# Kernel tuning notes

Measured on AMD Instinct MI355X. Metric: run time of the kernel, lower is better.

## Reference

```python
import jax, jax.numpy as jnp
import numpy as np

B, T, D = 16, 1024, 1024
H, HS = 16, 64  # num_heads, attention_head_size; H*HS == D
NEG_INF = -1e9


def setup_inputs() -> dict:
    key = jax.random.key(0)
    ks = jax.random.split(key, 6)
    s = 0.02
    x = jax.random.normal(ks[0], (B, T, D), dtype=jnp.float32)
    Wq = jax.random.normal(ks[1], (D, HS), dtype=jnp.float32) * s
    Wk = jax.random.normal(ks[2], (D, HS), dtype=jnp.float32) * s
    Wv = jax.random.normal(ks[3], (D, HS), dtype=jnp.float32) * s
    Wp = jax.random.normal(ks[4], (D, D), dtype=jnp.float32) * s
    bp = jax.random.normal(ks[5], (D,), dtype=jnp.float32) * s
    return {"x": x, "Wq": Wq, "Wk": Wk, "Wv": Wv, "Wp": Wp, "bp": bp}


def reference(x, Wq, Wk, Wv, Wp, bp):
    # Single shared Head (ModuleList([Head(...)] * num_heads) shares weights).
    q = jnp.einsum('btd,dh->bth', x, Wq)  # [B,T,HS]
    k = jnp.einsum('btd,dh->bth', x, Wk)
    v = jnp.einsum('btd,dh->bth', x, Wv)
    scale = 1.0 / jnp.sqrt(jnp.float32(HS))
    scores = jnp.einsum('bth,bsh->bts', q, k) * scale  # [B,T,T]
    causal = jnp.tril(jnp.ones((T, T), dtype=bool))
    scores = jnp.where(causal[None, :, :], scores, NEG_INF)
    attn = jax.nn.softmax(scores, axis=-1)
    head_out = jnp.einsum('bts,bsh->bth', attn, v)  # [B,T,HS]
    # Concatenate H identical head outputs along feature dim -> [B,T,D]
    out = jnp.tile(head_out, (1, 1, H))
    out = jnp.einsum('btd,de->bte', out, Wp) + bp
    return out
```

## Files before the change

### kernel.cpp

```cpp
#include <hip/hip_runtime.h>
#include <hip/hip_bf16.h>
#include <cstddef>

typedef __attribute__((ext_vector_type(8))) __bf16 bf16x8;
typedef __attribute__((ext_vector_type(4))) float f32x4;

static __device__ __forceinline__ unsigned short f2bf(float f) {
    __bf16 h = (__bf16)f;
    return __builtin_bit_cast(unsigned short, h);
}

__global__ void prep_weights(const float* __restrict__ Wq, const float* __restrict__ Wk,
                             const float* __restrict__ Wv, const float* __restrict__ Wp,
                             unsigned short* __restrict__ Wfrag,
                             unsigned short* __restrict__ WpFrag) {
    int blk = blockIdx.x;
    if (blk < 768) {
        int idx = blk * 256 + threadIdx.x;
        int CB = idx >> 14;
        int rem = idx & 16383;
        int S = rem >> 9;
        int r2 = rem & 511;
        int l = r2 >> 3, j = r2 & 7;
        int col = CB * 16 + (l & 15);
        int k = S * 32 + (l >> 4) * 8 + j;
        float v;
        if (col < 64)       v = Wq[k * 64 + col];
        else if (col < 128) v = Wk[k * 64 + (col - 64)];
        else                v = Wv[k * 64 + (col - 128)];
        Wfrag[idx] = f2bf(v);
    } else {
        int idx = (blk - 768) * 256 + threadIdx.x;
        int CB = idx >> 10;
        int rem = idx & 1023;
        int s = rem >> 9;
        int r2 = rem & 511;
        int l = r2 >> 3, j = r2 & 7;
        int col = CB * 16 + (l & 15);
        int h = s * 32 + (l >> 4) * 8 + j;
        float sum = 0.f;
#pragma unroll
        for (int j16 = 0; j16 < 16; ++j16) sum += Wp[(size_t)(j16 * 64 + h) * 1024 + col];
        WpFrag[idx] = f2bf(sum);
    }
}

__global__ __launch_bounds__(256) void qkv_gemm(const float* __restrict__ x,
                                                const unsigned short* __restrict__ Wfrag,
                                                unsigned short* __restrict__ qs,
                                                unsigned short* __restrict__ ks,
                                                unsigned short* __restrict__ vT) {
    __shared__ __align__(16) unsigned short xl[2][16 * 128];

    const int tid = threadIdx.x;
    const int lane = tid & 63;
    const int w = tid >> 6;
    const int g = lane >> 4, c = lane & 15;
    const int row0 = blockIdx.x * 16;

    const int srow = tid >> 4;
    const int scolf = (tid & 15) * 8;
    const float* xsrc = x + (size_t)(row0 + srow) * 1024 + scolf;
    const int sdst = srow * 256 + ((scolf * 2) ^ ((srow & 7) << 4));

    const unsigned short* wbase = Wfrag + (size_t)(w * 3) * 32 * 512 + lane * 8;

    f32x4 acc[3];
#pragma unroll
    for (int cb = 0; cb < 3; ++cb) acc[cb] = (f32x4){0.f, 0.f, 0.f, 0.f};

    float4 pre0[2], pre1[2];
    pre0[0] = *(const float4*)(xsrc);
    pre0[1] = *(const float4*)(xsrc + 4);
    pre1[0] = *(const float4*)(xsrc + 128);
    pre1[1] = *(const float4*)(xsrc + 132);

    bf16x8 bP[3][6];
#pragma unroll
    for (int pp = 0; pp < 2; ++pp) {
#pragma unroll
        for (int i = 0; i < 6; ++i) {
            int SB = pp * 2 + (i / 3);
            int cb = i % 3;
            bP[pp][i] = *(const bf16x8*)(wbase + ((size_t)(cb * 32 + SB) * 512));
        }
    }

    {
        bf16x8 vv;
        vv[0] = (__bf16)pre0[0].x; vv[1] = (__bf16)pre0[0].y; vv[2] = (__bf16)pre0[0].z; vv[3] = (__bf16)pre0[0].w;
        vv[4] = (__bf16)pre0[1].x; vv[5] = (__bf16)pre0[1].y; vv[6] = (__bf16)pre0[1].z; vv[7] = (__bf16)pre0[1].w;
        *(bf16x8*)((char*)xl[0] + sdst) = vv;
    }
    __syncthreads();

#pragma unroll
    for (int p = 0; p < 16; ++p) {
        const int t = p >> 1;
        if ((p & 1) == 0 && t + 2 < 8) {
            if ((t & 1) == 0) {
                pre0[0] = *(const float4*)(xsrc + (t + 2) * 128);
                pre0[1] = *(const float4*)(xsrc + (t + 2) * 128 + 4);
            } else {
                pre1[0] = *(const float4*)(xsrc + (t + 2) * 128);
                pre1[1] = *(const float4*)(xsrc + (t + 2) * 128 + 4);
            }
        }
        if (p + 2 < 16) {
#pragma unroll
            for (int i = 0; i < 6; ++i) {
                int SB = (p + 2) * 2 + (i / 3);
                int cb = i % 3;
                bP[(p + 2) % 3][i] = *(const bf16x8*)(wbase + ((size_t)(cb * 32 + SB) * 512));
            }
        }
#pragma unroll
        for (int sl = 0; sl < 2; ++sl) {
            int s = (p & 1) * 2 + sl;
            bf16x8 af = *(const bf16x8*)((char*)xl[t & 1] + c * 256 +
                                         ((s * 64 + g * 16) ^ ((c & 7) << 4)));
#pragma unroll
            for (int cb = 0; cb < 3; ++cb)
                acc[cb] = __builtin_amdgcn_mfma_f32_16x16x32_bf16(af, bP[p % 3][sl * 3 + cb], acc[cb], 0, 0, 0);
        }
        if (p & 1) {
            if (t < 7) {
                bf16x8 vv;
                if ((t & 1) == 0) {
                    vv[0] = (__bf16)pre1[0].x; vv[1] = (__bf16)pre1[0].y; vv[2] = (__bf16)pre1[0].z; vv[3] = (__bf16)pre1[0].w;
                    vv[4] = (__bf16)pre1[1].x; vv[5] = (__bf16)pre1[1].y; vv[6] = (__bf16)pre1[1].z; vv[7] = (__bf16)pre1[1].w;
                    *(bf16x8*)((char*)xl[1] + sdst) = vv;
                } else {
                    vv[0] = (__bf16)pre0[0].x; vv[1] = (__bf16)pre0[0].y; vv[2] = (__bf16)pre0[0].z; vv[3] = (__bf16)pre0[0].w;
                    vv[4] = (__bf16)pre0[1].x; vv[5] = (__bf16)pre0[1].y; vv[6] = (__bf16)pre0[1].z; vv[7] = (__bf16)pre0[1].w;
                    *(bf16x8*)((char*)xl[0] + sdst) = vv;
                }
            }
            __syncthreads();
        }
    }

    const float QSCALE = 0.125f * 1.44269504088896340736f;
#pragma unroll
    for (int cb = 0; cb < 3; ++cb) {
        int col = w * 48 + cb * 16 + c;
        int rowb = row0 + g * 4;
        if (col < 64) {
#pragma unroll
            for (int r = 0; r < 4; ++r)
                qs[(size_t)(rowb + r) * 64 + col] = f2bf(acc[cb][r] * QSCALE);
        } else if (col < 128) {
#pragma unroll
            for (int r = 0; r < 4; ++r)
                ks[(size_t)(rowb + r) * 64 + (col - 64)] = f2bf(acc[cb][r]);
        } else {
            int h = col - 128;
            int b = rowb >> 10, trow = rowb & 1023;
            unsigned long long dv =
                (unsigned long long)f2bf(acc[cb][0]) |
                ((unsigned long long)f2bf(acc[cb][1]) << 16) |
                ((unsigned long long)f2bf(acc[cb][2]) << 32) |
                ((unsigned long long)f2bf(acc[cb][3]) << 48);
            *(unsigned long long*)(vT + (size_t)b * 65536 + (size_t)h * 1024 + trow) = dv;
        }
    }
}

__global__ __launch_bounds__(256) void attn_proj(const unsigned short* __restrict__ qs,
                                                 const unsigned short* __restrict__ ks,
                                                 const unsigned short* __restrict__ vT,
                                                 const unsigned short* __restrict__ WpFrag,
                                                 const float* __restrict__ bp,
                                                 float* __restrict__ out) {
    __shared__ unsigned short Plds[4][16 * 40];
    __shared__ float oL[3][1024];
    __shared__ float pL[3][256];
    __shared__ __align__(16) unsigned short hl[16 * 64];

    const int tid = threadIdx.x;
    const int lane = tid & 63;
    const int q4 = tid >> 6;
    const int g = lane >> 4, c = lane & 15;

    const int tau = blockIdx.x;
    const int b = tau & 15;
    const int qidx = 63 - (tau >> 4);
    const int qr0 = qidx * 16;
    const int qend = qr0 + 16;
    const int nc = (qidx >> 1) + 1;
    const int c0 = (q4 * nc) >> 2;
    const int c1 = ((q4 + 1) * nc) >> 2;

    const unsigned short* qbase = qs + ((size_t)b * 1024 + qr0 + c) * 64 + g * 8;
    bf16x8 aq0 = *(const bf16x8*)(qbase);
    bf16x8 aq1 = *(const bf16x8*)(qbase + 32);

    const unsigned short* kB = ks + (size_t)b * 1024 * 64;
    const unsigned short* vB = vT + (size_t)b * 64 * 1024;

    f32x4 o[4];
#pragma unroll
    for (int i = 0; i < 4; ++i) o[i] = (f32x4){0.f, 0.f, 0.f, 0.f};
    float psum[4] = {0.f, 0.f, 0.f, 0.f};
    const f32x4 zero = {0.f, 0.f, 0.f, 0.f};

    bf16x8 kc0, kc1, kc2, kc3, vc0, vc1, vc2, vc3;
    if (c0 < c1) {
        const unsigned short* kp = kB + (size_t)(c0 * 32 + c) * 64 + g * 8;
        kc0 = *(const bf16x8*)(kp);
        kc1 = *(const bf16x8*)(kp + 32);
        kc2 = *(const bf16x8*)(kp + 16 * 64);
        kc3 = *(const bf16x8*)(kp + 16 * 64 + 32);
        const unsigned short* vp = vB + (size_t)c * 1024 + c0 * 32 + g * 8;
        vc0 = *(const bf16x8*)(vp);
        vc1 = *(const bf16x8*)(vp + 16 * 1024);
        vc2 = *(const bf16x8*)(vp + 32 * 1024);
        vc3 = *(const bf16x8*)(vp + 48 * 1024);
    }

    for (int ci = c0; ci < c1; ++ci) {
        const int j0 = ci * 32;
        const bool full = (j0 + 16 < qend);
        f32x4 s0 = __builtin_amdgcn_mfma_f32_16x16x32_bf16(aq0, kc0, zero, 0, 0, 0);
        s0 = __builtin_amdgcn_mfma_f32_16x16x32_bf16(aq1, kc1, s0, 0, 0, 0);
        f32x4 s1 = zero;
        if (full) {
            s1 = __builtin_amdgcn_mfma_f32_16x16x32_bf16(aq0, kc2, zero, 0, 0, 0);
            s1 = __builtin_amdgcn_mfma_f32_16x16x32_bf16(aq1, kc3, s1, 0, 0, 0);
        }

        bf16x8 kn0, kn1, kn2, kn3, vn0, vn1, vn2, vn3;
        if (ci + 1 < c1) {
            const int jn = (ci + 1) * 32;
            const unsigned short* kp = kB + (size_t)(jn + c) * 64 + g * 8;
            kn0 = *(const bf16x8*)(kp);
            kn1 = *(const bf16x8*)(kp + 32);
            kn2 = *(const bf16x8*)(kp + 16 * 64);
            kn3 = *(const bf16x8*)(kp + 16 * 64 + 32);
            const unsigned short* vp = vB + (size_t)c * 1024 + jn + g * 8;
            vn0 = *(const bf16x8*)(vp);
            vn1 = *(const bf16x8*)(vp + 16 * 1024);
            vn2 = *(const bf16x8*)(vp + 32 * 1024);
            vn3 = *(const bf16x8*)(vp + 48 * 1024);
        }

#pragma unroll
        for (int r = 0; r < 4; ++r) {
            int t = qr0 + g * 4 + r;
            float e0 = (j0 + c > t) ? 0.f : exp2f(s0[r]);
            float e1 = (!full || j0 + 16 + c > t) ? 0.f : exp2f(s1[r]);
            psum[r] += e0 + e1;
            Plds[q4][(g * 4 + r) * 40 + c]      = f2bf(e0);
            Plds[q4][(g * 4 + r) * 40 + 16 + c] = f2bf(e1);
        }
        bf16x8 pa = *(const bf16x8*)(&Plds[q4][c * 40 + g * 8]);
        o[0] = __builtin_amdgcn_mfma_f32_16x16x32_bf16(pa, vc0, o[0], 0, 0, 0);
        o[1] = __builtin_amdgcn_mfma_f32_16x16x32_bf16(pa, vc1, o[1], 0, 0, 0);
        o[2] = __builtin_amdgcn_mfma_f32_16x16x32_bf16(pa, vc2, o[2], 0, 0, 0);
        o[3] = __builtin_amdgcn_mfma_f32_16x16x32_bf16(pa, vc3, o[3], 0, 0, 0);

        kc0 = kn0; kc1 = kn1; kc2 = kn2; kc3 = kn3;
        vc0 = vn0; vc1 = vn1; vc2 = vn2; vc3 = vn3;
    }

    if (q4 != 0) {
#pragma unroll
        for (int hb = 0; hb < 4; ++hb)
            *(f32x4*)&oL[q4 - 1][(hb * 64 + lane) * 4] = o[hb];
        f32x4 pv = {psum[0], psum[1], psum[2], psum[3]};
        *(f32x4*)&pL[q4 - 1][lane * 4] = pv;
    }
    __syncthreads();
    if (q4 == 0) {
#pragma unroll
        for (int part = 0; part < 3; ++part) {
            f32x4 pv = *(const f32x4*)&pL[part][lane * 4];
#pragma unroll
            for (int r = 0; r < 4; ++r) psum[r] += pv[r];
#pragma unroll
            for (int hb = 0; hb < 4; ++hb) {
                f32x4 po = *(const f32x4*)&oL[part][(hb * 64 + lane) * 4];
#pragma unroll
                for (int r = 0; r < 4; ++r) o[hb][r] += po[r];
            }
        }
        float inv[4];
#pragma unroll
        for (int r = 0; r < 4; ++r) {
            float ps = psum[r];
            ps += __shfl_xor(ps, 1);
            ps += __shfl_xor(ps, 2);
            ps += __shfl_xor(ps, 4);
            ps += __shfl_xor(ps, 8);
            inv[r] = 1.f / ps;
        }
#pragma unroll
        for (int hb = 0; hb < 4; ++hb) {
#pragma unroll
            for (int r = 0; r < 4; ++r) {
                int row = g * 4 + r;
                int colb = (hb * 16 + c) * 2;
                *(unsigned short*)((char*)hl + row * 128 + (colb ^ ((row & 7) << 4))) =
                    f2bf(o[hb][r] * inv[r]);
            }
        }
    }
    __syncthreads();

    bf16x8 a0 = *(const bf16x8*)((char*)hl + c * 128 + ((g * 16) ^ ((c & 7) << 4)));
    bf16x8 a1 = *(const bf16x8*)((char*)hl + c * 128 + ((64 + g * 16) ^ ((c & 7) << 4)));
    const size_t obase = ((size_t)b * 1024 + qr0) * 1024;
#pragma unroll
    for (int cb = 0; cb < 16; ++cb) {
        int CB = q4 * 16 + cb;
        bf16x8 b0 = *(const bf16x8*)(WpFrag + (size_t)(CB * 2 + 0) * 512 + lane * 8);
        bf16x8 b1 = *(const bf16x8*)(WpFrag + (size_t)(CB * 2 + 1) * 512 + lane * 8);
        f32x4 acc = __builtin_amdgcn_mfma_f32_16x16x32_bf16(a0, b0, zero, 0, 0, 0);
        acc = __builtin_amdgcn_mfma_f32_16x16x32_bf16(a1, b1, acc, 0, 0, 0);
        int col = CB * 16 + c;
        float bias = bp[col];
#pragma unroll
        for (int r = 0; r < 4; ++r) {
            out[obase + (size_t)(g * 4 + r) * 1024 + col] = acc[r] + bias;
        }
    }
}

extern "C" void kernel_launch(void* const* d_in, const int* in_sizes, int n_in,
                              void* d_out, int out_size, void* d_ws, size_t ws_size,
                              hipStream_t stream) {
    (void)in_sizes; (void)n_in; (void)out_size; (void)ws_size;
    const float* x  = (const float*)d_in[0];
    const float* Wq = (const float*)d_in[1];
    const float* Wk = (const float*)d_in[2];
    const float* Wv = (const float*)d_in[3];
    const float* Wp = (const float*)d_in[4];
    const float* bp = (const float*)d_in[5];
    float* out = (float*)d_out;

    const size_t NTOK = 16 * 1024;
    unsigned short* ws = (unsigned short*)d_ws;
    unsigned short* qs     = ws;
    unsigned short* ks     = qs + NTOK * 64;
    unsigned short* vT     = ks + NTOK * 64;
    unsigned short* Wfrag  = vT + NTOK * 64;
    unsigned short* WpFrag = Wfrag + 192 * 1024;

    prep_weights<<<1024, 256, 0, stream>>>(Wq, Wk, Wv, Wp, Wfrag, WpFrag);
    qkv_gemm<<<1024, 256, 0, stream>>>(x, Wfrag, qs, ks, vT);
    attn_proj<<<1024, 256, 0, stream>>>(qs, ks, vT, WpFrag, bp, out);
}
```

Baseline: 63.24 us.

## Process two row tiles per block in QKV GEMM and attention-projection kernels

The QKV GEMM now computes 32 rows per block, so each weight fragment loaded from global memory feeds two MFMA row tiles, and the grid is halved. The attention kernel now handles two query tiles (two batches, same query index) per block with two waves each instead of four waves on one tile. This lets each Wp fragment be reused for two output tiles in the projection. The intent is to cut redundant weight loads and the cross-wave reduction overhead. In exchange each tile's KV loop is split across only two waves, and register and LDS use per block rise.

```diff
diff --git a/kernel.cpp b/kernel.cpp
--- a/kernel.cpp
+++ b/kernel.cpp
@@ -50,30 +50,33 @@
                                                 unsigned short* __restrict__ qs,
                                                 unsigned short* __restrict__ ks,
                                                 unsigned short* __restrict__ vT) {
-    __shared__ __align__(16) unsigned short xl[2][16 * 128];
+    __shared__ __align__(16) unsigned short xl[2][32 * 128];
 
     const int tid = threadIdx.x;
     const int lane = tid & 63;
     const int w = tid >> 6;
     const int g = lane >> 4, c = lane & 15;
-    const int row0 = blockIdx.x * 16;
-
-    const int srow = tid >> 4;
-    const int scolf = (tid & 15) * 8;
+    const int row0 = blockIdx.x * 32;
+
+    const int srow = tid >> 3;
+    const int scolf = (tid & 7) * 16;
     const float* xsrc = x + (size_t)(row0 + srow) * 1024 + scolf;
-    const int sdst = srow * 256 + ((scolf * 2) ^ ((srow & 7) << 4));
+    const int sdst0 = srow * 256 + ((scolf * 2) ^ ((srow & 7) << 4));
+    const int sdst1 = srow * 256 + ((scolf * 2 + 16) ^ ((srow & 7) << 4));
 
     const unsigned short* wbase = Wfrag + (size_t)(w * 3) * 32 * 512 + lane * 8;
 
-    f32x4 acc[3];
-#pragma unroll
-    for (int cb = 0; cb < 3; ++cb) acc[cb] = (f32x4){0.f, 0.f, 0.f, 0.f};
-
-    float4 pre0[2], pre1[2];
-    pre0[0] = *(const float4*)(xsrc);
-    pre0[1] = *(const float4*)(xsrc + 4);
-    pre1[0] = *(const float4*)(xsrc + 128);
-    pre1[1] = *(const float4*)(xsrc + 132);
+    f32x4 acc[2][3];
+#pragma unroll
+    for (int mr = 0; mr < 2; ++mr)
+#pragma unroll
+        for (int cb = 0; cb < 3; ++cb) acc[mr][cb] = (f32x4){0.f, 0.f, 0.f, 0.f};
+
+    float4 pre0[4], pre1[4];
+#pragma unroll
+    for (int i = 0; i < 4; ++i) pre0[i] = *(const float4*)(xsrc + i * 4);
+#pragma unroll
+    for (int i = 0; i < 4; ++i) pre1[i] = *(const float4*)(xsrc + 128 + i * 4);
 
     bf16x8 bP[3][6];
 #pragma unroll
@@ -87,10 +90,13 @@
     }
 
     {
-        bf16x8 vv;
-        vv[0] = (__bf16)pre0[0].x; vv[1] = (__bf16)pre0[0].y; vv[2] = (__bf16)pre0[0].z; vv[3] = (__bf16)pre0[0].w;
-        vv[4] = (__bf16)pre0[1].x; vv[5] = (__bf16)pre0[1].y; vv[6] = (__bf16)pre0[1].z; vv[7] = (__bf16)pre0[1].w;
-        *(bf16x8*)((char*)xl[0] + sdst) = vv;
+        bf16x8 v0, v1;
+#pragma unroll
+        for (int j = 0; j < 4; ++j) { v0[j] = (__bf16)pre0[0][j]; v0[4 + j] = (__bf16)pre0[1][j]; }
+#pragma unroll
+        for (int j = 0; j < 4; ++j) { v1[j] = (__bf16)pre0[2][j]; v1[4 + j] = (__bf16)pre0[3][j]; }
+        *(bf16x8*)((char*)xl[0] + sdst0) = v0;
+        *(bf16x8*)((char*)xl[0] + sdst1) = v1;
     }
     __syncthreads();
 
@@ -99,11 +105,11 @@
         const int t = p >> 1;
         if ((p & 1) == 0 && t + 2 < 8) {
             if ((t & 1) == 0) {
-                pre0[0] = *(const float4*)(xsrc + (t + 2) * 128);
-                pre0[1] = *(const float4*)(xsrc + (t + 2) * 128 + 4);
+#pragma unroll
+                for (int i = 0; i < 4; ++i) pre0[i] = *(const float4*)(xsrc + (t + 2) * 128 + i * 4);
             } else {
-                pre1[0] = *(const float4*)(xsrc + (t + 2) * 128);
-                pre1[1] = *(const float4*)(xsrc + (t + 2) * 128 + 4);
+#pragma unroll
+                for (int i = 0; i < 4; ++i) pre1[i] = *(const float4*)(xsrc + (t + 2) * 128 + i * 4);
             }
         }
         if (p + 2 < 16) {
@@ -117,23 +123,34 @@
 #pragma unroll
         for (int sl = 0; sl < 2; ++sl) {
             int s = (p & 1) * 2 + sl;
-            bf16x8 af = *(const bf16x8*)((char*)xl[t & 1] + c * 256 +
-                                         ((s * 64 + g * 16) ^ ((c & 7) << 4)));
-#pragma unroll
-            for (int cb = 0; cb < 3; ++cb)
-                acc[cb] = __builtin_amdgcn_mfma_f32_16x16x32_bf16(af, bP[p % 3][sl * 3 + cb], acc[cb], 0, 0, 0);
+            bf16x8 af[2];
+#pragma unroll
+            for (int mr = 0; mr < 2; ++mr)
+                af[mr] = *(const bf16x8*)((char*)xl[t & 1] + (mr * 16 + c) * 256 +
+                                          ((s * 64 + g * 16) ^ ((c & 7) << 4)));
+#pragma unroll
+            for (int cb = 0; cb < 3; ++cb) {
+                acc[0][cb] = __builtin_amdgcn_mfma_f32_16x16x32_bf16(af[0], bP[p % 3][sl * 3 + cb], acc[0][cb], 0, 0, 0);
+                acc[1][cb] = __builtin_amdgcn_mfma_f32_16x16x32_bf16(af[1], bP[p % 3][sl * 3 + cb], acc[1][cb], 0, 0, 0);
+            }
         }
         if (p & 1) {
             if (t < 7) {
-                bf16x8 vv;
+                bf16x8 v0, v1;
                 if ((t & 1) == 0) {
-                    vv[0] = (__bf16)pre1[0].x; vv[1] = (__bf16)pre1[0].y; vv[2] = (__bf16)pre1[0].z; vv[3] = (__bf16)pre1[0].w;
-                    vv[4] = (__bf16)pre1[1].x; vv[5] = (__bf16)pre1[1].y; vv[6] = (__bf16)pre1[1].z; vv[7] = (__bf16)pre1[1].w;
-                    *(bf16x8*)((char*)xl[1] + sdst) = vv;
+#pragma unroll
+                    for (int j = 0; j < 4; ++j) { v0[j] = (__bf16)pre1[0][j]; v0[4 + j] = (__bf16)pre1[1][j]; }
+#pragma unroll
+                    for (int j = 0; j < 4; ++j) { v1[j] = (__bf16)pre1[2][j]; v1[4 + j] = (__bf16)pre1[3][j]; }
+                    *(bf16x8*)((char*)xl[1] + sdst0) = v0;
+                    *(bf16x8*)((char*)xl[1] + sdst1) = v1;
                 } else {
-                    vv[0] = (__bf16)pre0[0].x; vv[1] = (__bf16)pre0[0].y; vv[2] = (__bf16)pre0[0].z; vv[3] = (__bf16)pre0[0].w;
-                    vv[4] = (__bf16)pre0[1].x; vv[5] = (__bf16)pre0[1].y; vv[6] = (__bf16)pre0[1].z; vv[7] = (__bf16)pre0[1].w;
-                    *(bf16x8*)((char*)xl[0] + sdst) = vv;
+#pragma unroll
+                    for (int j = 0; j < 4; ++j) { v0[j] = (__bf16)pre0[0][j]; v0[4 + j] = (__bf16)pre0[1][j]; }
+#pragma unroll
+                    for (int j = 0; j < 4; ++j) { v1[j] = (__bf16)pre0[2][j]; v1[4 + j] = (__bf16)pre0[3][j]; }
+                    *(bf16x8*)((char*)xl[0] + sdst0) = v0;
+                    *(bf16x8*)((char*)xl[0] + sdst1) = v1;
                 }
             }
             __syncthreads();
@@ -142,26 +159,29 @@
 
     const float QSCALE = 0.125f * 1.44269504088896340736f;
 #pragma unroll
-    for (int cb = 0; cb < 3; ++cb) {
-        int col = w * 48 + cb * 16 + c;
-        int rowb = row0 + g * 4;
-        if (col < 64) {
-#pragma unroll
-            for (int r = 0; r < 4; ++r)
-                qs[(size_t)(rowb + r) * 64 + col] = f2bf(acc[cb][r] * QSCALE);
-        } else if (col < 128) {
-#pragma unroll
-            for (int r = 0; r < 4; ++r)
-                ks[(size_t)(rowb + r) * 64 + (col - 64)] = f2bf(acc[cb][r]);
-        } else {
-            int h = col - 128;
-            int b = rowb >> 10, trow = rowb & 1023;
-            unsigned long long dv =
-                (unsigned long long)f2bf(acc[cb][0]) |
-                ((unsigned long long)f2bf(acc[cb][1]) << 16) |
-                ((unsigned long long)f2bf(acc[cb][2]) << 32) |
-                ((unsigned long long)f2bf(acc[cb][3]) << 48);
-            *(unsigned long long*)(vT + (size_t)b * 65536 + (size_t)h * 1024 + trow) = dv;
+    for (int mr = 0; mr < 2; ++mr) {
+#pragma unroll
+        for (int cb = 0; cb < 3; ++cb) {
+            int col = w * 48 + cb * 16 + c;
+            int rowb = row0 + mr * 16 + g * 4;
+            if (col < 64) {
+#pragma unroll
+                for (int r = 0; r < 4; ++r)
+                    qs[(size_t)(rowb + r) * 64 + col] = f2bf(acc[mr][cb][r] * QSCALE);
+            } else if (col < 128) {
+#pragma unroll
+                for (int r = 0; r < 4; ++r)
+                    ks[(size_t)(rowb + r) * 64 + (col - 64)] = f2bf(acc[mr][cb][r]);
+            } else {
+                int h = col - 128;
+                int bb = rowb >> 10, trow = rowb & 1023;
+                unsigned long long dv =
+                    (unsigned long long)f2bf(acc[mr][cb][0]) |
+                    ((unsigned long long)f2bf(acc[mr][cb][1]) << 16) |
+                    ((unsigned long long)f2bf(acc[mr][cb][2]) << 32) |
+                    ((unsigned long long)f2bf(acc[mr][cb][3]) << 48);
+                *(unsigned long long*)(vT + (size_t)bb * 65536 + (size_t)h * 1024 + trow) = dv;
+            }
         }
     }
 }
@@ -173,30 +193,32 @@
                                                  const float* __restrict__ bp,
                                                  float* __restrict__ out) {
     __shared__ unsigned short Plds[4][16 * 40];
-    __shared__ float oL[3][1024];
-    __shared__ float pL[3][256];
-    __shared__ __align__(16) unsigned short hl[16 * 64];
+    __shared__ float oL[2][1024];
+    __shared__ float pL[2][256];
+    __shared__ __align__(16) unsigned short hl[2][16 * 64];
 
     const int tid = threadIdx.x;
     const int lane = tid & 63;
-    const int q4 = tid >> 6;
+    const int wid = tid >> 6;
+    const int tslot = wid >> 1;
+    const int half = wid & 1;
     const int g = lane >> 4, c = lane & 15;
 
-    const int tau = blockIdx.x;
-    const int b = tau & 15;
+    const int tau = blockIdx.x * 2 + tslot;
+    const int bb = tau & 15;
     const int qidx = 63 - (tau >> 4);
     const int qr0 = qidx * 16;
     const int qend = qr0 + 16;
     const int nc = (qidx >> 1) + 1;
-    const int c0 = (q4 * nc) >> 2;
-    const int c1 = ((q4 + 1) * nc) >> 2;
-
-    const unsigned short* qbase = qs + ((size_t)b * 1024 + qr0 + c) * 64 + g * 8;
+    const int c0 = half ? (nc >> 1) : 0;
+    const int c1 = half ? nc : (nc >> 1);
+
+    const unsigned short* qbase = qs + ((size_t)bb * 1024 + qr0 + c) * 64 + g * 8;
     bf16x8 aq0 = *(const bf16x8*)(qbase);
     bf16x8 aq1 = *(const bf16x8*)(qbase + 32);
 
-    const unsigned short* kB = ks + (size_t)b * 1024 * 64;
-    const unsigned short* vB = vT + (size_t)b * 64 * 1024;
+    const unsigned short* kB = ks + (size_t)bb * 1024 * 64;
+    const unsigned short* vB = vT + (size_t)bb * 64 * 1024;
 
     f32x4 o[4];
 #pragma unroll
@@ -250,10 +272,10 @@
             float e0 = (j0 + c > t) ? 0.f : exp2f(s0[r]);
             float e1 = (!full || j0 + 16 + c > t) ? 0.f : exp2f(s1[r]);
             psum[r] += e0 + e1;
-            Plds[q4][(g * 4 + r) * 40 + c]      = f2bf(e0);
-            Plds[q4][(g * 4 + r) * 40 + 16 + c] = f2bf(e1);
-        }
-        bf16x8 pa = *(const bf16x8*)(&Plds[q4][c * 40 + g * 8]);
+            Plds[wid][(g * 4 + r) * 40 + c]      = f2bf(e0);
+            Plds[wid][(g * 4 + r) * 40 + 16 + c] = f2bf(e1);
+        }
+        bf16x8 pa = *(const bf16x8*)(&Plds[wid][c * 40 + g * 8]);
         o[0] = __builtin_amdgcn_mfma_f32_16x16x32_bf16(pa, vc0, o[0], 0, 0, 0);
         o[1] = __builtin_amdgcn_mfma_f32_16x16x32_bf16(pa, vc1, o[1], 0, 0, 0);
         o[2] = __builtin_amdgcn_mfma_f32_16x16x32_bf16(pa, vc2, o[2], 0, 0, 0);
@@ -263,31 +285,20 @@
         vc0 = vn0; vc1 = vn1; vc2 = vn2; vc3 = vn3;
     }
 
-    if (q4 != 0) {
+    if (half == 1) {
 #pragma unroll
         for (int hb = 0; hb < 4; ++hb)
-            *(f32x4*)&oL[q4 - 1][(hb * 64 + lane) * 4] = o[hb];
+            *(f32x4*)&oL[tslot][(hb * 64 + lane) * 4] = o[hb];
         f32x4 pv = {psum[0], psum[1], psum[2], psum[3]};
-        *(f32x4*)&pL[q4 - 1][lane * 4] = pv;
+        *(f32x4*)&pL[tslot][lane * 4] = pv;
     }
     __syncthreads();
-    if (q4 == 0) {
-#pragma unroll
-        for (int part = 0; part < 3; ++part) {
-            f32x4 pv = *(const f32x4*)&pL[part][lane * 4];
-#pragma unroll
-            for (int r = 0; r < 4; ++r) psum[r] += pv[r];
-#pragma unroll
-            for (int hb = 0; hb < 4; ++hb) {
-                f32x4 po = *(const f32x4*)&oL[part][(hb * 64 + lane) * 4];
-#pragma unroll
-                for (int r = 0; r < 4; ++r) o[hb][r] += po[r];
-            }
-        }
+    if (half == 0) {
+        f32x4 pv = *(const f32x4*)&pL[tslot][lane * 4];
         float inv[4];
 #pragma unroll
         for (int r = 0; r < 4; ++r) {
-            float ps = psum[r];
+            float ps = psum[r] + pv[r];
             ps += __shfl_xor(ps, 1);
             ps += __shfl_xor(ps, 2);
             ps += __shfl_xor(ps, 4);
@@ -296,32 +307,41 @@
         }
 #pragma unroll
         for (int hb = 0; hb < 4; ++hb) {
+            f32x4 po = *(const f32x4*)&oL[tslot][(hb * 64 + lane) * 4];
 #pragma unroll
             for (int r = 0; r < 4; ++r) {
                 int row = g * 4 + r;
                 int colb = (hb * 16 + c) * 2;
-                *(unsigned short*)((char*)hl + row * 128 + (colb ^ ((row & 7) << 4))) =
-                    f2bf(o[hb][r] * inv[r]);
+                *(unsigned short*)((char*)hl[tslot] + row * 128 + (colb ^ ((row & 7) << 4))) =
+                    f2bf((o[hb][r] + po[r]) * inv[r]);
             }
         }
     }
     __syncthreads();
 
-    bf16x8 a0 = *(const bf16x8*)((char*)hl + c * 128 + ((g * 16) ^ ((c & 7) << 4)));
-    bf16x8 a1 = *(const bf16x8*)((char*)hl + c * 128 + ((64 + g * 16) ^ ((c & 7) << 4)));
-    const size_t obase = ((size_t)b * 1024 + qr0) * 1024;
+    bf16x8 a0t0 = *(const bf16x8*)((char*)hl[0] + c * 128 + ((g * 16) ^ ((c & 7) << 4)));
+    bf16x8 a1t0 = *(const bf16x8*)((char*)hl[0] + c * 128 + ((64 + g * 16) ^ ((c & 7) << 4)));
+    bf16x8 a0t1 = *(const bf16x8*)((char*)hl[1] + c * 128 + ((g * 16) ^ ((c & 7) << 4)));
+    bf16x8 a1t1 = *(const bf16x8*)((char*)hl[1] + c * 128 + ((64 + g * 16) ^ ((c & 7) << 4)));
+    const int b0 = (blockIdx.x * 2) & 15;
+    const int b1 = (blockIdx.x * 2 + 1) & 15;
+    const size_t obase0 = ((size_t)b0 * 1024 + qr0) * 1024;
+    const size_t obase1 = ((size_t)b1 * 1024 + qr0) * 1024;
 #pragma unroll
     for (int cb = 0; cb < 16; ++cb) {
-        int CB = q4 * 16 + cb;
-        bf16x8 b0 = *(const bf16x8*)(WpFrag + (size_t)(CB * 2 + 0) * 512 + lane * 8);
-        bf16x8 b1 = *(const bf16x8*)(WpFrag + (size_t)(CB * 2 + 1) * 512 + lane * 8);
-        f32x4 acc = __builtin_amdgcn_mfma_f32_16x16x32_bf16(a0, b0, zero, 0, 0, 0);
-        acc = __builtin_amdgcn_mfma_f32_16x16x32_bf16(a1, b1, acc, 0, 0, 0);
+        int CB = wid * 16 + cb;
+        bf16x8 wb0 = *(const bf16x8*)(WpFrag + (size_t)(CB * 2 + 0) * 512 + lane * 8);
+        bf16x8 wb1 = *(const bf16x8*)(WpFrag + (size_t)(CB * 2 + 1) * 512 + lane * 8);
+        f32x4 acc0 = __builtin_amdgcn_mfma_f32_16x16x32_bf16(a0t0, wb0, zero, 0, 0, 0);
+        acc0 = __builtin_amdgcn_mfma_f32_16x16x32_bf16(a1t0, wb1, acc0, 0, 0, 0);
+        f32x4 acc1 = __builtin_amdgcn_mfma_f32_16x16x32_bf16(a0t1, wb0, zero, 0, 0, 0);
+        acc1 = __builtin_amdgcn_mfma_f32_16x16x32_bf16(a1t1, wb1, acc1, 0, 0, 0);
         int col = CB * 16 + c;
         float bias = bp[col];
 #pragma unroll
         for (int r = 0; r < 4; ++r) {
-            out[obase + (size_t)(g * 4 + r) * 1024 + col] = acc[r] + bias;
+            out[obase0 + (size_t)(g * 4 + r) * 1024 + col] = acc0[r] + bias;
+            out[obase1 + (size_t)(g * 4 + r) * 1024 + col] = acc1[r] + bias;
         }
     }
 }
@@ -347,6 +367,6 @@
     unsigned short* WpFrag = Wfrag + 192 * 1024;
 
     prep_weights<<<1024, 256, 0, stream>>>(Wq, Wk, Wv, Wp, Wfrag, WpFrag);
-    qkv_gemm<<<1024, 256, 0, stream>>>(x, Wfrag, qs, ks, vT);
-    attn_proj<<<1024, 256, 0, stream>>>(qs, ks, vT, WpFrag, bp, out);
-}
+    qkv_gemm<<<512, 256, 0, stream>>>(x, Wfrag, qs, ks, vT);
+    attn_proj<<<512, 256, 0, stream>>>(qs, ks, vT, WpFrag, bp, out);
+}
```

Measured after the change: 56.95 us. 1.11x faster.
